# Kernel optimization log

Measured on AMD Instinct MI355X. Metric: run time of the kernel, lower is better.

Reference implementation:

```python
import jax, jax.numpy as jnp
import numpy as np

NATOMS = 50000   # total atoms in batch
NCONF = 500      # number of configurations (atoms_per_structure.size)
NPAIRS = 1_000_000  # neighbor pairs; 3*NPAIRS derivative rows (x,y,z)
ND = 55          # descriptor length (SNAP twojmax=8)
H = 64           # MLP hidden width


def setup_inputs() -> dict:
    key = jax.random.key(0)
    ks = jax.random.split(key, 10)
    nrows = 3 * NPAIRS
    x = jax.random.normal(ks[0], (NATOMS, ND), dtype=jnp.float32)
    xd = jax.random.normal(ks[1], (nrows, ND), dtype=jnp.float32)
    # sorted config index per atom: 100 atoms per config
    indices = jnp.repeat(jnp.arange(NCONF, dtype=jnp.int32), NATOMS // NCONF)
    atoms_per_structure = jnp.full((NCONF,), NATOMS // NCONF, dtype=jnp.int32)
    types = jnp.zeros((NATOMS,), dtype=jnp.int32)  # unused for multi_element_option==1
    # xd_indx: col0 = atom index whose dE/dD row is gathered, col2 = cartesian dim
    neigh_i = jax.random.randint(ks[2], (nrows,), 0, NATOMS, dtype=jnp.int32)
    dims = jnp.tile(jnp.arange(3, dtype=jnp.int32), NPAIRS)
    xd_indx = jnp.stack([neigh_i, jnp.zeros_like(neigh_i), dims], axis=1)
    unique_j = jax.random.randint(ks[3], (nrows,), 0, NATOMS, dtype=jnp.int32)
    # MLP parameters (network_architecture0): 55 -> 64 -> 64 -> 1, tanh
    W1 = jax.random.normal(ks[4], (ND, H), dtype=jnp.float32) / np.float32(np.sqrt(ND))
    b1 = jnp.zeros((H,), dtype=jnp.float32)
    W2 = jax.random.normal(ks[5], (H, H), dtype=jnp.float32) / np.float32(np.sqrt(H))
    b2 = jnp.zeros((H,), dtype=jnp.float32)
    W3 = jax.random.normal(ks[6], (H, 1), dtype=jnp.float32) / np.float32(np.sqrt(H))
    b3 = jnp.zeros((1,), dtype=jnp.float32)
    return {
        "x": x, "xd": xd, "indices": indices,
        "atoms_per_structure": atoms_per_structure, "types": types,
        "xd_indx": xd_indx, "unique_j": unique_j,
        "W1": W1, "b1": b1, "W2": W2, "b2": b2, "W3": W3, "b3": b3,
    }


def reference(x, xd, indices, atoms_per_structure, types, xd_indx, unique_j,
              W1, b1, W2, b2, W3, b3):
    def mlp(xx):  # [N, ND] -> [N, 1] per-atom energies
        h = jnp.tanh(xx @ W1 + b1)
        h = jnp.tanh(h @ W2 + b2)
        return h @ W3 + b3

    # per-atom energies and dE/dD via vjp (== autograd.grad with ones cotangent)
    per_atom_energies, vjp_fn = jax.vjp(mlp, x)
    dEdD = vjp_fn(jnp.ones_like(per_atom_energies))[0]  # [NATOMS, ND]

    # energy: index_add per-atom energies into per-config totals
    predicted_energy_total = jax.ops.segment_sum(
        per_atom_energies[:, 0], indices, num_segments=NCONF)

    # forces: gather dEdD rows, elementwise multiply with dD/dR, reduce over ND,
    # scatter-add into atom j / cartesian-dim slots. Output layout matches
    # torch.flatten(cat([fx, fy, fz], dim=1)) == index 3*j + dim.
    contrib = jnp.sum(xd * dEdD[xd_indx[:, 0]], axis=1)  # [3*NPAIRS]
    seg = unique_j * 3 + xd_indx[:, 2]
    predicted_forces = jax.ops.segment_sum(contrib, seg, num_segments=3 * NATOMS)

    return predicted_energy_total, predicted_forces
```

## Files before the change

kernel.cpp:

```cpp
#include <hip/hip_runtime.h>

constexpr int kNAtoms = 50000;
constexpr int kNConf  = 500;
constexpr int kNRows  = 3000000;
constexpr int kND     = 55;
constexpr int kNDP    = 56;
constexpr int kH      = 64;
constexpr int kOutN   = kNConf + 3 * kNAtoms;

__global__ void zero_out_kernel(float* __restrict__ out, int n) {
  int i = blockIdx.x * blockDim.x + threadIdx.x;
  if (i < n) out[i] = 0.0f;
}

__global__ __launch_bounds__(128)
void mlp_kernel(const float* __restrict__ x,
                const int* __restrict__ indices,
                const float* __restrict__ W1, const float* __restrict__ b1,
                const float* __restrict__ W2, const float* __restrict__ b2,
                const float* __restrict__ W3, const float* __restrict__ b3,
                float* __restrict__ out_energy,
                float* __restrict__ dEdD) {
  __shared__ float sW1[kND * kH];
  __shared__ float sW2[kH * kH];
  __shared__ float sW2T[kH * kH];
  __shared__ float sW3[kH];
  __shared__ float sb1[kH];
  __shared__ float sb2[kH];
  __shared__ float sb3s;

  const int t = threadIdx.x;
  for (int i = t; i < kND * kH; i += 128) sW1[i] = W1[i];
  for (int i = t; i < kH * kH; i += 128) sW2[i] = W2[i];
  for (int i = t; i < kH * kH; i += 128) {
    int k = i / kH, j = i % kH;
    sW2T[i] = W2[j * kH + k];
  }
  if (t < kH) { sW3[t] = W3[t]; sb1[t] = b1[t]; sb2[t] = b2[t]; }
  if (t == 0) sb3s = b3[0];
  __syncthreads();

  const int atom = blockIdx.x * 128 + t;
  if (atom >= kNAtoms) return;

  float xv[kND];
  #pragma unroll
  for (int d = 0; d < kND; ++d) xv[d] = x[atom * kND + d];

  float h1[kH];
  #pragma unroll
  for (int k = 0; k < kH; k += 4) {
    float s0 = sb1[k+0], s1 = sb1[k+1], s2 = sb1[k+2], s3 = sb1[k+3];
    #pragma unroll
    for (int d = 0; d < kND; ++d) {
      const float xvd = xv[d];
      const float* w = &sW1[d * kH + k];
      s0 += xvd * w[0]; s1 += xvd * w[1]; s2 += xvd * w[2]; s3 += xvd * w[3];
    }
    h1[k+0] = tanhf(s0); h1[k+1] = tanhf(s1);
    h1[k+2] = tanhf(s2); h1[k+3] = tanhf(s3);
  }

  float da2[kH];
  float energy = sb3s;
  #pragma unroll
  for (int k = 0; k < kH; k += 4) {
    float s0 = sb2[k+0], s1 = sb2[k+1], s2 = sb2[k+2], s3 = sb2[k+3];
    #pragma unroll
    for (int j = 0; j < kH; ++j) {
      const float hj = h1[j];
      const float* w = &sW2[j * kH + k];
      s0 += hj * w[0]; s1 += hj * w[1]; s2 += hj * w[2]; s3 += hj * w[3];
    }
    const float t0 = tanhf(s0), t1 = tanhf(s1), t2 = tanhf(s2), t3 = tanhf(s3);
    energy += t0 * sW3[k+0] + t1 * sW3[k+1] + t2 * sW3[k+2] + t3 * sW3[k+3];
    da2[k+0] = sW3[k+0] * (1.0f - t0 * t0);
    da2[k+1] = sW3[k+1] * (1.0f - t1 * t1);
    da2[k+2] = sW3[k+2] * (1.0f - t2 * t2);
    da2[k+3] = sW3[k+3] * (1.0f - t3 * t3);
  }

  atomicAdd(&out_energy[indices[atom]], energy);

  float da1[kH];
  #pragma unroll
  for (int j = 0; j < kH; j += 4) {
    float s0 = 0.f, s1 = 0.f, s2 = 0.f, s3 = 0.f;
    #pragma unroll
    for (int k = 0; k < kH; ++k) {
      const float g = da2[k];
      const float* w = &sW2T[k * kH + j];
      s0 += g * w[0]; s1 += g * w[1]; s2 += g * w[2]; s3 += g * w[3];
    }
    const float t0 = h1[j+0], t1 = h1[j+1], t2 = h1[j+2], t3 = h1[j+3];
    da1[j+0] = s0 * (1.0f - t0 * t0);
    da1[j+1] = s1 * (1.0f - t1 * t1);
    da1[j+2] = s2 * (1.0f - t2 * t2);
    da1[j+3] = s3 * (1.0f - t3 * t3);
  }

  float dE[kND];
  #pragma unroll
  for (int d = 0; d < kND; ++d) dE[d] = 0.f;
  #pragma unroll
  for (int j = 0; j < kH; j += 4) {
    const float g0 = da1[j+0], g1 = da1[j+1], g2 = da1[j+2], g3 = da1[j+3];
    #pragma unroll
    for (int d = 0; d < kND; ++d) {
      const float* w = &sW1[d * kH + j];
      dE[d] += g0 * w[0] + g1 * w[1] + g2 * w[2] + g3 * w[3];
    }
  }
  #pragma unroll
  for (int d = 0; d < kND; ++d) dEdD[(size_t)atom * kNDP + d] = dE[d];
}

constexpr int kFB = 128;
__global__ __launch_bounds__(kFB)
void forces_kernel(const float* __restrict__ xd,
                   const int* __restrict__ xd_indx,
                   const int* __restrict__ unique_j,
                   const float* __restrict__ dEdD,
                   float* __restrict__ out_forces) {
  __shared__ float sxd[kFB * kND];
  const int t = threadIdx.x;
  const int base = blockIdx.x * kFB;
  const int n = min(kFB, kNRows - base);

  {
    const int nfl = n * kND;
    const int nf4 = nfl >> 2;
    const float4* __restrict__ src4 =
        reinterpret_cast<const float4*>(xd + (size_t)base * kND);
    float4* __restrict__ dst4 = reinterpret_cast<float4*>(sxd);
    for (int i = t; i < nf4; i += kFB) dst4[i] = src4[i];
    for (int i = (nf4 << 2) + t; i < nfl; i += kFB)
      sxd[i] = xd[(size_t)base * kND + i];
  }
  __syncthreads();

  if (t >= n) return;
  const int r   = base + t;
  const int ai  = xd_indx[3 * r + 0];
  const int dim = xd_indx[3 * r + 2];
  const int j   = unique_j[r];

  const float* __restrict__ xr = &sxd[t * kND];
  const float* __restrict__ gr = dEdD + (size_t)ai * kNDP;
  const float4* __restrict__ g4 = reinterpret_cast<const float4*>(gr);

  float s = 0.f;
  #pragma unroll
  for (int q = 0; q < 13; ++q) {
    const float4 g = g4[q];
    s += xr[4*q+0] * g.x + xr[4*q+1] * g.y + xr[4*q+2] * g.z + xr[4*q+3] * g.w;
  }
  s += xr[52] * gr[52] + xr[53] * gr[53] + xr[54] * gr[54];

  atomicAdd(&out_forces[3 * j + dim], s);
}

extern "C" void kernel_launch(void* const* d_in, const int* in_sizes, int n_in,
                              void* d_out, int out_size, void* d_ws, size_t ws_size,
                              hipStream_t stream) {
  const float* x        = (const float*)d_in[0];
  const float* xd       = (const float*)d_in[1];
  const int*   indices  = (const int*)d_in[2];
  const int*   xd_indx  = (const int*)d_in[5];
  const int*   unique_j = (const int*)d_in[6];
  const float* W1 = (const float*)d_in[7];
  const float* b1 = (const float*)d_in[8];
  const float* W2 = (const float*)d_in[9];
  const float* b2 = (const float*)d_in[10];
  const float* W3 = (const float*)d_in[11];
  const float* b3 = (const float*)d_in[12];

  float* out  = (float*)d_out;
  float* dEdD = (float*)d_ws;

  zero_out_kernel<<<(kOutN + 255) / 256, 256, 0, stream>>>(out, kOutN);
  mlp_kernel<<<(kNAtoms + 127) / 128, 128, 0, stream>>>(
      x, indices, W1, b1, W2, b2, W3, b3, out, dEdD);
  forces_kernel<<<(kNRows + kFB - 1) / kFB, kFB, 0, stream>>>(
      xd, xd_indx, unique_j, dEdD, out + kNConf);
}
```

Measured before the change: 1.173 ms.

## Tile MLP as shared-memory register-blocked GEMMs and prefetch gathered dEdD rows

The MLP kernel changes from one atom per thread with huge register arrays to 64-atom tiles per 256-thread block. Each thread computes a 4x4 register block of every layer's matrix product from shared memory, using vector loads and a shuffle reduction for the energies. The forces kernel issues its dEdD gather and index loads before the xd staging copy so their latency overlaps, and it reads the streaming inputs with nontemporal loads. This removes register spilling in the MLP, at the cost of more shared memory per block and extra barriers, and raises register use in the forces kernel.

```diff
diff --git a/kernel.cpp b/kernel.cpp
--- a/kernel.cpp
+++ b/kernel.cpp
@@ -1,11 +1,12 @@
 #include <hip/hip_runtime.h>
+
+typedef float f4v __attribute__((ext_vector_type(4)));
 
 constexpr int kNAtoms = 50000;
 constexpr int kNConf  = 500;
 constexpr int kNRows  = 3000000;
 constexpr int kND     = 55;
 constexpr int kNDP    = 56;
-constexpr int kH      = 64;
 constexpr int kOutN   = kNConf + 3 * kNAtoms;
 
 __global__ void zero_out_kernel(float* __restrict__ out, int n) {
@@ -13,7 +14,8 @@
   if (i < n) out[i] = 0.0f;
 }
 
-__global__ __launch_bounds__(128)
+constexpr int kTS = 68;
+__global__ __launch_bounds__(256)
 void mlp_kernel(const float* __restrict__ x,
                 const int* __restrict__ indices,
                 const float* __restrict__ W1, const float* __restrict__ b1,
@@ -21,98 +23,180 @@
                 const float* __restrict__ W3, const float* __restrict__ b3,
                 float* __restrict__ out_energy,
                 float* __restrict__ dEdD) {
-  __shared__ float sW1[kND * kH];
-  __shared__ float sW2[kH * kH];
-  __shared__ float sW2T[kH * kH];
-  __shared__ float sW3[kH];
-  __shared__ float sb1[kH];
-  __shared__ float sb2[kH];
-  __shared__ float sb3s;
-
-  const int t = threadIdx.x;
-  for (int i = t; i < kND * kH; i += 128) sW1[i] = W1[i];
-  for (int i = t; i < kH * kH; i += 128) sW2[i] = W2[i];
-  for (int i = t; i < kH * kH; i += 128) {
-    int k = i / kH, j = i % kH;
-    sW2T[i] = W2[j * kH + k];
-  }
-  if (t < kH) { sW3[t] = W3[t]; sb1[t] = b1[t]; sb2[t] = b2[t]; }
-  if (t == 0) sb3s = b3[0];
-  __syncthreads();
-
-  const int atom = blockIdx.x * 128 + t;
-  if (atom >= kNAtoms) return;
-
-  float xv[kND];
-  #pragma unroll
-  for (int d = 0; d < kND; ++d) xv[d] = x[atom * kND + d];
-
-  float h1[kH];
-  #pragma unroll
-  for (int k = 0; k < kH; k += 4) {
-    float s0 = sb1[k+0], s1 = sb1[k+1], s2 = sb1[k+2], s3 = sb1[k+3];
-    #pragma unroll
-    for (int d = 0; d < kND; ++d) {
-      const float xvd = xv[d];
-      const float* w = &sW1[d * kH + k];
-      s0 += xvd * w[0]; s1 += xvd * w[1]; s2 += xvd * w[2]; s3 += xvd * w[3];
-    }
-    h1[k+0] = tanhf(s0); h1[k+1] = tanhf(s1);
-    h1[k+2] = tanhf(s2); h1[k+3] = tanhf(s3);
-  }
-
-  float da2[kH];
-  float energy = sb3s;
-  #pragma unroll
-  for (int k = 0; k < kH; k += 4) {
-    float s0 = sb2[k+0], s1 = sb2[k+1], s2 = sb2[k+2], s3 = sb2[k+3];
-    #pragma unroll
-    for (int j = 0; j < kH; ++j) {
-      const float hj = h1[j];
-      const float* w = &sW2[j * kH + k];
-      s0 += hj * w[0]; s1 += hj * w[1]; s2 += hj * w[2]; s3 += hj * w[3];
-    }
-    const float t0 = tanhf(s0), t1 = tanhf(s1), t2 = tanhf(s2), t3 = tanhf(s3);
-    energy += t0 * sW3[k+0] + t1 * sW3[k+1] + t2 * sW3[k+2] + t3 * sW3[k+3];
-    da2[k+0] = sW3[k+0] * (1.0f - t0 * t0);
-    da2[k+1] = sW3[k+1] * (1.0f - t1 * t1);
-    da2[k+2] = sW3[k+2] * (1.0f - t2 * t2);
-    da2[k+3] = sW3[k+3] * (1.0f - t3 * t3);
-  }
-
-  atomicAdd(&out_energy[indices[atom]], energy);
-
-  float da1[kH];
-  #pragma unroll
-  for (int j = 0; j < kH; j += 4) {
-    float s0 = 0.f, s1 = 0.f, s2 = 0.f, s3 = 0.f;
-    #pragma unroll
-    for (int k = 0; k < kH; ++k) {
-      const float g = da2[k];
-      const float* w = &sW2T[k * kH + j];
-      s0 += g * w[0]; s1 += g * w[1]; s2 += g * w[2]; s3 += g * w[3];
-    }
-    const float t0 = h1[j+0], t1 = h1[j+1], t2 = h1[j+2], t3 = h1[j+3];
-    da1[j+0] = s0 * (1.0f - t0 * t0);
-    da1[j+1] = s1 * (1.0f - t1 * t1);
-    da1[j+2] = s2 * (1.0f - t2 * t2);
-    da1[j+3] = s3 * (1.0f - t3 * t3);
-  }
-
-  float dE[kND];
-  #pragma unroll
-  for (int d = 0; d < kND; ++d) dE[d] = 0.f;
-  #pragma unroll
-  for (int j = 0; j < kH; j += 4) {
-    const float g0 = da1[j+0], g1 = da1[j+1], g2 = da1[j+2], g3 = da1[j+3];
-    #pragma unroll
-    for (int d = 0; d < kND; ++d) {
-      const float* w = &sW1[d * kH + j];
-      dE[d] += g0 * w[0] + g1 * w[1] + g2 * w[2] + g3 * w[3];
-    }
-  }
-  #pragma unroll
-  for (int d = 0; d < kND; ++d) dEdD[(size_t)atom * kNDP + d] = dE[d];
+  __shared__ float sX[64 * kTS];
+  __shared__ float sH1[64 * kTS];
+  __shared__ float sDa2[64 * kTS];
+  __shared__ float sW1v[56 * 64];
+  __shared__ float sW1T[64 * 64];
+  __shared__ float sW2v[64 * 64];
+  __shared__ float sW2T[64 * 64];
+  __shared__ float sW3v[64], sb1v[64], sb2v[64];
+
+  const int t  = threadIdx.x;
+  const int tb = t & 15;
+  const int ta = t >> 4;
+  const int a0 = blockIdx.x * 64;
+
+  for (int i = t; i < 56 * 64; i += 256) sW1v[i] = (i < 55 * 64) ? W1[i] : 0.0f;
+  for (int i = t; i < 64 * 64; i += 256) {
+    int j = i >> 6, d = i & 63;
+    sW1T[i] = (d < 55) ? W1[d * 64 + j] : 0.0f;
+  }
+  for (int i = t; i < 64 * 64; i += 256) sW2v[i] = W2[i];
+  for (int i = t; i < 64 * 64; i += 256) {
+    int k = i >> 6, j = i & 63;
+    sW2T[i] = W2[j * 64 + k];
+  }
+  if (t < 64) { sW3v[t] = W3[t]; sb1v[t] = b1[t]; sb2v[t] = b2[t]; }
+  for (int i = t; i < 64 * 55; i += 256) {
+    int r = i / 55, c = i % 55;
+    int atom = a0 + r;
+    sX[r * kTS + c] = (atom < kNAtoms) ? x[(size_t)atom * kND + c] : 0.0f;
+  }
+  if (t < 64) sX[t * kTS + 55] = 0.0f;
+  const float b3v = b3[0];
+  __syncthreads();
+
+  float acc[4][4];
+  #pragma unroll
+  for (int i = 0; i < 4; ++i)
+    #pragma unroll
+    for (int q = 0; q < 4; ++q) acc[i][q] = sb1v[tb * 4 + q];
+  #pragma unroll 2
+  for (int dq = 0; dq < 14; ++dq) {
+    const int d0 = dq * 4;
+    const f4v bv0 = *(const f4v*)&sW1v[(d0 + 0) * 64 + tb * 4];
+    const f4v bv1 = *(const f4v*)&sW1v[(d0 + 1) * 64 + tb * 4];
+    const f4v bv2 = *(const f4v*)&sW1v[(d0 + 2) * 64 + tb * 4];
+    const f4v bv3 = *(const f4v*)&sW1v[(d0 + 3) * 64 + tb * 4];
+    #pragma unroll
+    for (int i = 0; i < 4; ++i) {
+      const f4v av = *(const f4v*)&sX[(ta * 4 + i) * kTS + d0];
+      #pragma unroll
+      for (int q = 0; q < 4; ++q)
+        acc[i][q] += av[0] * bv0[q] + av[1] * bv1[q]
+                   + av[2] * bv2[q] + av[3] * bv3[q];
+    }
+  }
+  #pragma unroll
+  for (int i = 0; i < 4; ++i) {
+    f4v hv;
+    #pragma unroll
+    for (int q = 0; q < 4; ++q) hv[q] = tanhf(acc[i][q]);
+    *(f4v*)&sH1[(ta * 4 + i) * kTS + tb * 4] = hv;
+  }
+  __syncthreads();
+
+  #pragma unroll
+  for (int i = 0; i < 4; ++i)
+    #pragma unroll
+    for (int q = 0; q < 4; ++q) acc[i][q] = sb2v[tb * 4 + q];
+  #pragma unroll 2
+  for (int jq = 0; jq < 16; ++jq) {
+    const int j0 = jq * 4;
+    const f4v bv0 = *(const f4v*)&sW2v[(j0 + 0) * 64 + tb * 4];
+    const f4v bv1 = *(const f4v*)&sW2v[(j0 + 1) * 64 + tb * 4];
+    const f4v bv2 = *(const f4v*)&sW2v[(j0 + 2) * 64 + tb * 4];
+    const f4v bv3 = *(const f4v*)&sW2v[(j0 + 3) * 64 + tb * 4];
+    #pragma unroll
+    for (int i = 0; i < 4; ++i) {
+      const f4v av = *(const f4v*)&sH1[(ta * 4 + i) * kTS + j0];
+      #pragma unroll
+      for (int q = 0; q < 4; ++q)
+        acc[i][q] += av[0] * bv0[q] + av[1] * bv1[q]
+                   + av[2] * bv2[q] + av[3] * bv3[q];
+    }
+  }
+  float epart[4];
+  {
+    const f4v w3 = *(const f4v*)&sW3v[tb * 4];
+    #pragma unroll
+    for (int i = 0; i < 4; ++i) {
+      f4v dv; float e = 0.0f;
+      #pragma unroll
+      for (int q = 0; q < 4; ++q) {
+        const float h2 = tanhf(acc[i][q]);
+        e += h2 * w3[q];
+        dv[q] = w3[q] * (1.0f - h2 * h2);
+      }
+      epart[i] = e;
+      *(f4v*)&sDa2[(ta * 4 + i) * kTS + tb * 4] = dv;
+    }
+  }
+  #pragma unroll
+  for (int off = 8; off >= 1; off >>= 1)
+    #pragma unroll
+    for (int i = 0; i < 4; ++i) epart[i] += __shfl_xor(epart[i], off, 16);
+  if (tb == 0) {
+    #pragma unroll
+    for (int i = 0; i < 4; ++i) {
+      const int atom = a0 + ta * 4 + i;
+      if (atom < kNAtoms)
+        atomicAdd(&out_energy[indices[atom]], epart[i] + b3v);
+    }
+  }
+  __syncthreads();
+
+  #pragma unroll
+  for (int i = 0; i < 4; ++i)
+    #pragma unroll
+    for (int q = 0; q < 4; ++q) acc[i][q] = 0.0f;
+  #pragma unroll 2
+  for (int kq = 0; kq < 16; ++kq) {
+    const int k0 = kq * 4;
+    const f4v bv0 = *(const f4v*)&sW2T[(k0 + 0) * 64 + tb * 4];
+    const f4v bv1 = *(const f4v*)&sW2T[(k0 + 1) * 64 + tb * 4];
+    const f4v bv2 = *(const f4v*)&sW2T[(k0 + 2) * 64 + tb * 4];
+    const f4v bv3 = *(const f4v*)&sW2T[(k0 + 3) * 64 + tb * 4];
+    #pragma unroll
+    for (int i = 0; i < 4; ++i) {
+      const f4v av = *(const f4v*)&sDa2[(ta * 4 + i) * kTS + k0];
+      #pragma unroll
+      for (int q = 0; q < 4; ++q)
+        acc[i][q] += av[0] * bv0[q] + av[1] * bv1[q]
+                   + av[2] * bv2[q] + av[3] * bv3[q];
+    }
+  }
+  #pragma unroll
+  for (int i = 0; i < 4; ++i) {
+    const f4v hv = *(const f4v*)&sH1[(ta * 4 + i) * kTS + tb * 4];
+    f4v dv;
+    #pragma unroll
+    for (int q = 0; q < 4; ++q) dv[q] = acc[i][q] * (1.0f - hv[q] * hv[q]);
+    *(f4v*)&sX[(ta * 4 + i) * kTS + tb * 4] = dv;
+  }
+  __syncthreads();
+
+  #pragma unroll
+  for (int i = 0; i < 4; ++i)
+    #pragma unroll
+    for (int q = 0; q < 4; ++q) acc[i][q] = 0.0f;
+  #pragma unroll 2
+  for (int jq = 0; jq < 16; ++jq) {
+    const int j0 = jq * 4;
+    const f4v bv0 = *(const f4v*)&sW1T[(j0 + 0) * 64 + tb * 4];
+    const f4v bv1 = *(const f4v*)&sW1T[(j0 + 1) * 64 + tb * 4];
+    const f4v bv2 = *(const f4v*)&sW1T[(j0 + 2) * 64 + tb * 4];
+    const f4v bv3 = *(const f4v*)&sW1T[(j0 + 3) * 64 + tb * 4];
+    #pragma unroll
+    for (int i = 0; i < 4; ++i) {
+      const f4v av = *(const f4v*)&sX[(ta * 4 + i) * kTS + j0];
+      #pragma unroll
+      for (int q = 0; q < 4; ++q)
+        acc[i][q] += av[0] * bv0[q] + av[1] * bv1[q]
+                   + av[2] * bv2[q] + av[3] * bv3[q];
+    }
+  }
+  if (tb < 14) {
+    #pragma unroll
+    for (int i = 0; i < 4; ++i) {
+      const int atom = a0 + ta * 4 + i;
+      if (atom < kNAtoms) {
+        f4v ov; ov[0]=acc[i][0]; ov[1]=acc[i][1]; ov[2]=acc[i][2]; ov[3]=acc[i][3];
+        *(f4v*)&dEdD[(size_t)atom * kNDP + tb * 4] = ov;
+      }
+    }
+  }
 }
 
 constexpr int kFB = 128;
@@ -127,35 +211,42 @@
   const int base = blockIdx.x * kFB;
   const int n = min(kFB, kNRows - base);
 
+  int ai = 0, dim = 0, j = 0;
+  f4v g[14];
+  if (t < n) {
+    const int r = base + t;
+    ai  = __builtin_nontemporal_load(&xd_indx[3 * r + 0]);
+    dim = __builtin_nontemporal_load(&xd_indx[3 * r + 2]);
+    j   = __builtin_nontemporal_load(&unique_j[r]);
+    const f4v* __restrict__ g4 =
+        reinterpret_cast<const f4v*>(dEdD + (size_t)ai * kNDP);
+    #pragma unroll
+    for (int q = 0; q < 14; ++q) g[q] = g4[q];
+  }
+
   {
     const int nfl = n * kND;
     const int nf4 = nfl >> 2;
-    const float4* __restrict__ src4 =
-        reinterpret_cast<const float4*>(xd + (size_t)base * kND);
-    float4* __restrict__ dst4 = reinterpret_cast<float4*>(sxd);
-    for (int i = t; i < nf4; i += kFB) dst4[i] = src4[i];
+    const f4v* __restrict__ src4 =
+        reinterpret_cast<const f4v*>(xd + (size_t)base * kND);
+    f4v* __restrict__ dst4 = reinterpret_cast<f4v*>(sxd);
+    for (int i = t; i < nf4; i += kFB)
+      dst4[i] = __builtin_nontemporal_load(&src4[i]);
     for (int i = (nf4 << 2) + t; i < nfl; i += kFB)
-      sxd[i] = xd[(size_t)base * kND + i];
+      sxd[i] = __builtin_nontemporal_load(&xd[(size_t)base * kND + i]);
   }
   __syncthreads();
 
   if (t >= n) return;
-  const int r   = base + t;
-  const int ai  = xd_indx[3 * r + 0];
-  const int dim = xd_indx[3 * r + 2];
-  const int j   = unique_j[r];
-
   const float* __restrict__ xr = &sxd[t * kND];
-  const float* __restrict__ gr = dEdD + (size_t)ai * kNDP;
-  const float4* __restrict__ g4 = reinterpret_cast<const float4*>(gr);
-
-  float s = 0.f;
+
+  float s = 0.0f;
   #pragma unroll
   for (int q = 0; q < 13; ++q) {
-    const float4 g = g4[q];
-    s += xr[4*q+0] * g.x + xr[4*q+1] * g.y + xr[4*q+2] * g.z + xr[4*q+3] * g.w;
-  }
-  s += xr[52] * gr[52] + xr[53] * gr[53] + xr[54] * gr[54];
+    s += xr[4*q+0] * g[q][0] + xr[4*q+1] * g[q][1]
+       + xr[4*q+2] * g[q][2] + xr[4*q+3] * g[q][3];
+  }
+  s += xr[52] * g[13][0] + xr[53] * g[13][1] + xr[54] * g[13][2];
 
   atomicAdd(&out_forces[3 * j + dim], s);
 }
@@ -179,7 +270,7 @@
   float* dEdD = (float*)d_ws;
 
   zero_out_kernel<<<(kOutN + 255) / 256, 256, 0, stream>>>(out, kOutN);
-  mlp_kernel<<<(kNAtoms + 127) / 128, 128, 0, stream>>>(
+  mlp_kernel<<<(kNAtoms + 63) / 64, 256, 0, stream>>>(
       x, indices, W1, b1, W2, b2, W3, b3, out, dEdD);
   forces_kernel<<<(kNRows + kFB - 1) / kFB, kFB, 0, stream>>>(
       xd, xd_indx, unique_j, dEdD, out + kNConf);
```

After: 1.145 ms. 2.4% less time.
